# Optimization experiments

Hardware: AMD Instinct MI355X
Metric: run time of the kernel (lower is better)

## Reference

```python
import jax, jax.numpy as jnp
import numpy as np

N = 1_000_000
H = 256
DIMS = [1, H, H, H, H]
N_LAYERS = 4  # 4 linear layers, sin activation after the first 3


def setup_inputs() -> dict:
    key = jax.random.key(0)
    ks = jax.random.split(key, 1 + 2 * N_LAYERS)
    d = {"x": jax.random.normal(ks[0], (N, 2), dtype=jnp.float32)}
    i = 1
    for pre in ("x", "t"):
        for l in range(N_LAYERS):
            lim = 1.0 / np.sqrt(DIMS[l])  # torch.nn.Linear default init range
            d[f"{pre}W{l}"] = jax.random.uniform(
                ks[i], (DIMS[l], DIMS[l + 1]), dtype=jnp.float32, minval=-lim, maxval=lim)
            d[f"{pre}b{l}"] = jnp.zeros((DIMS[l + 1],), dtype=jnp.float32)
            i += 1
    return d


def _mlp(h, params):
    # params: list of (W, b); sin activation after all but the last layer
    n = len(params)
    for idx, (W, b) in enumerate(params):
        h = h @ W + b
        if idx < n - 1:
            h = jnp.sin(h)
    return h


def reference(x, xW0, xb0, xW1, xb1, xW2, xb2, xW3, xb3,
              tW0, tb0, tW1, tb1, tW2, tb2, tW3, tb3):
    x_params = [(xW0, xb0), (xW1, xb1), (xW2, xb2), (xW3, xb3)]
    t_params = [(tW0, tb0), (tW1, tb1), (tW2, tb2), (tW3, tb3)]
    nx = _mlp(x[:, 0:1], x_params)  # [N, H]
    nt = _mlp(x[:, 1:2], t_params)  # [N, H]
    # diag(A @ B.T) == rowwise dot product; avoids the O(N^2) matmul
    even = jnp.sum(nx[:, 0::2] * nt[:, 0::2], axis=-1)  # [N]
    odd = jnp.sum(nx[:, 1::2] * nt[:, 1::2], axis=-1)   # [N]
    return jnp.stack([even, odd], axis=-1)  # [N, 2]
```

## Files before the change

### kernel.cpp

```cpp
#include <hip/hip_runtime.h>


typedef _Float16 f16x8 __attribute__((ext_vector_type(8)));
typedef _Float16 f16x4 __attribute__((ext_vector_type(4)));
typedef float f32x4 __attribute__((ext_vector_type(4)));

__device__ __forceinline__ int hswz(int m, int kbyte) {
    return m * 512 + ((((kbyte >> 4) ^ (m & 7)) & 31) << 4) + (kbyte & 15);
}

__device__ __forceinline__ void barrier_lds() {
    asm volatile("s_waitcnt lgkmcnt(0)" ::: "memory");
    __builtin_amdgcn_s_barrier();
}

__global__ void prepack(const float* __restrict__ xW1, const float* __restrict__ xW2,
                        const float* __restrict__ xW3, const float* __restrict__ tW1,
                        const float* __restrict__ tW2, const float* __restrict__ tW3,
                        _Float16* __restrict__ dst)
{
    int g = blockIdx.x * 256 + threadIdx.x;
    int L = g >> 16;
    int r = g & 65535;
    int j    = r & 7;
    int ln   = (r >> 3) & 15;
    int quad = (r >> 7) & 3;
    int nhi  = (r >> 9) & 15;
    int ks   = (r >> 13) & 1;
    int c    = (r >> 14) & 3;
    const float* W;
    switch (L) {
        case 0: W = xW1; break;
        case 1: W = xW2; break;
        case 2: W = xW3; break;
        case 3: W = tW1; break;
        case 4: W = tW2; break;
        default: W = tW3; break;
    }
    int n = nhi * 16 + ln;
    int k = c * 64 + ks * 32 + quad * 8 + j;
    dst[g] = (_Float16)W[k * 256 + n];
}


__device__ __forceinline__ void layer0_scalar(
    float xv, const float* __restrict__ W0, const float* __restrict__ b0,
    _Float16* __restrict__ hb, int tid)
{
    int m = tid >> 2;
    int q = tid & 3;
#pragma unroll
    for (int g = 0; g < 8; ++g) {
        int n0 = q * 64 + g * 8;
        f16x8 hv;
#pragma unroll
        for (int e = 0; e < 8; ++e) {
            float z = fmaf(xv, W0[n0 + e], b0[n0 + e]);
            hv[e] = (_Float16)__sinf(z);
        }
        *(f16x8*)((char*)hb + hswz(m, n0 * 2)) = hv;
    }
}

template<bool WRITE_H, bool HAS_NEXT>
__device__ __forceinline__ void gemm_layer(
    const _Float16* __restrict__ Wl,
    const _Float16* __restrict__ Wnext,
    const float* __restrict__ bias,
    _Float16* __restrict__ hb,
    f32x4 acc[4][4], f16x8 afr[2][4],
    int lane, int ln, int quad, int wave)
{
    f32x4 zero = {0.f, 0.f, 0.f, 0.f};
#pragma unroll
    for (int i = 0; i < 4; ++i)
#pragma unroll
        for (int j = 0; j < 4; ++j)
            acc[i][j] = zero;

    const _Float16* abase = Wl + wave * 2048 + lane * 8;

#pragma unroll
    for (int g = 0; g < 8; ++g) {
        f16x8 bfr[4];
#pragma unroll
        for (int j = 0; j < 4; ++j)
            bfr[j] = *(const f16x8*)((const char*)hb +
                                     hswz(16 * j + ln, g * 64 + quad * 16));

        __builtin_amdgcn_s_setprio(1);
#pragma unroll
        for (int i = 0; i < 4; ++i)
#pragma unroll
            for (int j = 0; j < 4; ++j)
                acc[i][j] = __builtin_amdgcn_mfma_f32_16x16x32_f16(
                    afr[g & 1][i], bfr[j], acc[i][j], 0, 0, 0);
        __builtin_amdgcn_s_setprio(0);

        if (g < 6) {
#pragma unroll
            for (int i = 0; i < 4; ++i)
                afr[g & 1][i] = *(const f16x8*)(abase + (g + 2) * 8192 + i * 512);
        } else if (HAS_NEXT) {
#pragma unroll
            for (int i = 0; i < 4; ++i)
                afr[g & 1][i] = *(const f16x8*)(Wnext + (g - 6) * 8192 +
                                                wave * 2048 + lane * 8 + i * 512);
        }
    }

    barrier_lds();

    if (WRITE_H) {
#pragma unroll
        for (int i = 0; i < 4; ++i) {
            int nb = wave * 64 + 16 * i + quad * 4;
            f32x4 bv = *(const f32x4*)&bias[nb];
#pragma unroll
            for (int j = 0; j < 4; ++j) {
                f16x4 hv;
                hv[0] = (_Float16)__sinf(acc[i][j][0] + bv[0]);
                hv[1] = (_Float16)__sinf(acc[i][j][1] + bv[1]);
                hv[2] = (_Float16)__sinf(acc[i][j][2] + bv[2]);
                hv[3] = (_Float16)__sinf(acc[i][j][3] + bv[3]);
                *(f16x4*)((char*)hb + hswz(16 * j + ln, nb * 2)) = hv;
            }
        }
        barrier_lds();
    }
}

__global__ __launch_bounds__(256, 2)
void mlp_fused(const float* __restrict__ x,
               const float* __restrict__ xW0, const float* __restrict__ xb0,
               const float* __restrict__ xb1, const float* __restrict__ xb2,
               const float* __restrict__ xb3,
               const float* __restrict__ tW0, const float* __restrict__ tb0,
               const float* __restrict__ tb1, const float* __restrict__ tb2,
               const float* __restrict__ tb3,
               const _Float16* __restrict__ Wp,
               float* __restrict__ out)
{
    __shared__ __align__(16) _Float16 hbuf[64 * 256];
    __shared__ __align__(16) float    params[10 * 256];

    const int tid = threadIdx.x;
    const int lane = tid & 63;
    const int wave = tid >> 6;
    const int ln = lane & 15;
    const int quad = lane >> 4;
    const int row0 = blockIdx.x * 64;

    {
        const float* psrc[10] = {xW0, xb0, tW0, tb0, xb1, xb2, xb3, tb1, tb2, tb3};
#pragma unroll
        for (int s = 0; s < 10; ++s)
            params[s * 256 + tid] = psrc[s][tid];
    }
    const float2 xv2 = ((const float2*)x)[row0 + (tid >> 2)];

    f32x4 xacc[4][4], tacc[4][4];
    f16x8 afr[2][4];

#pragma unroll
    for (int s = 0; s < 2; ++s)
#pragma unroll
        for (int i = 0; i < 4; ++i)
            afr[s][i] = *(const f16x8*)(Wp + s * 8192 + wave * 2048 +
                                        lane * 8 + i * 512);
    barrier_lds();

    layer0_scalar(xv2.x, &params[0], &params[256], hbuf, tid);
    barrier_lds();

    gemm_layer<true , true >(Wp + 0 * 65536, Wp + 1 * 65536, &params[4 * 256],
                             hbuf, xacc, afr, lane, ln, quad, wave);
    gemm_layer<true , true >(Wp + 1 * 65536, Wp + 2 * 65536, &params[5 * 256],
                             hbuf, xacc, afr, lane, ln, quad, wave);
    gemm_layer<false, true >(Wp + 2 * 65536, Wp + 3 * 65536, nullptr,
                             hbuf, xacc, afr, lane, ln, quad, wave);

    layer0_scalar(xv2.y, &params[2 * 256], &params[3 * 256], hbuf, tid);
    barrier_lds();

    gemm_layer<true , true >(Wp + 3 * 65536, Wp + 4 * 65536, &params[7 * 256],
                             hbuf, tacc, afr, lane, ln, quad, wave);
    gemm_layer<true , true >(Wp + 4 * 65536, Wp + 5 * 65536, &params[8 * 256],
                             hbuf, tacc, afr, lane, ln, quad, wave);
    gemm_layer<false, false>(Wp + 5 * 65536, nullptr, nullptr,
                             hbuf, tacc, afr, lane, ln, quad, wave);

    const float* xb3l = &params[6 * 256];
    const float* tb3l = &params[9 * 256];
    float ev[4] = {0.f, 0.f, 0.f, 0.f};
    float od[4] = {0.f, 0.f, 0.f, 0.f};
#pragma unroll
    for (int i = 0; i < 4; ++i) {
        int nb = wave * 64 + 16 * i + quad * 4;
        f32x4 xb = *(const f32x4*)&xb3l[nb];
        f32x4 tb = *(const f32x4*)&tb3l[nb];
#pragma unroll
        for (int j = 0; j < 4; ++j) {
            float a0 = xacc[i][j][0] + xb[0], c0 = tacc[i][j][0] + tb[0];
            float a1 = xacc[i][j][1] + xb[1], c1 = tacc[i][j][1] + tb[1];
            float a2 = xacc[i][j][2] + xb[2], c2 = tacc[i][j][2] + tb[2];
            float a3 = xacc[i][j][3] + xb[3], c3 = tacc[i][j][3] + tb[3];
            ev[j] += a0 * c0 + a2 * c2;
            od[j] += a1 * c1 + a3 * c3;
        }
    }
#pragma unroll
    for (int j = 0; j < 4; ++j) {
        ev[j] += __shfl_xor(ev[j], 16, 64);
        ev[j] += __shfl_xor(ev[j], 32, 64);
        od[j] += __shfl_xor(od[j], 16, 64);
        od[j] += __shfl_xor(od[j], 32, 64);
    }

    float* red = (float*)hbuf;
    if (lane < 16) {
#pragma unroll
        for (int j = 0; j < 4; ++j) {
            red[wave * 128 + j * 32 + lane * 2 + 0] = ev[j];
            red[wave * 128 + j * 32 + lane * 2 + 1] = od[j];
        }
    }
    __syncthreads();
    if (tid < 128) {
        int jj = tid >> 5, m16 = (tid >> 1) & 15, p = tid & 1;
        int base = jj * 32 + m16 * 2 + p;
        float s = red[base] + red[128 + base] + red[256 + base] + red[384 + base];
        out[(row0 + 16 * jj + m16) * 2 + p] = s;
    }
}

extern "C" void kernel_launch(void* const* d_in, const int* in_sizes, int n_in,
                              void* d_out, int out_size, void* d_ws, size_t ws_size,
                              hipStream_t stream)
{
    const float* x   = (const float*)d_in[0];
    const float* xW0 = (const float*)d_in[1];
    const float* xb0 = (const float*)d_in[2];
    const float* xW1 = (const float*)d_in[3];
    const float* xb1 = (const float*)d_in[4];
    const float* xW2 = (const float*)d_in[5];
    const float* xb2 = (const float*)d_in[6];
    const float* xW3 = (const float*)d_in[7];
    const float* xb3 = (const float*)d_in[8];
    const float* tW0 = (const float*)d_in[9];
    const float* tb0 = (const float*)d_in[10];
    const float* tW1 = (const float*)d_in[11];
    const float* tb1 = (const float*)d_in[12];
    const float* tW2 = (const float*)d_in[13];
    const float* tb2 = (const float*)d_in[14];
    const float* tW3 = (const float*)d_in[15];
    const float* tb3 = (const float*)d_in[16];

    _Float16* Wp = (_Float16*)d_ws;
    const int N = in_sizes[0] / 2;

    prepack<<<1536, 256, 0, stream>>>(xW1, xW2, xW3, tW1, tW2, tW3, Wp);
    mlp_fused<<<N / 64, 256, 0, stream>>>(x, xW0, xb0, xb1, xb2, xb3,
                                          tW0, tb0, tb1, tb2, tb3,
                                          Wp, (float*)d_out);
}
```

Baseline: 870.4 us.

## Interleave x and t MLP chains with double-buffered LDS to overlap sin epilogues

The two independent MLP chains are interleaved layer by layer, with the activation buffer double-buffered in LDS. While one chain's GEMM runs on the MFMA units, the other chain's bias+sin epilogue (or its scalar layer-0) is computed and written to the second buffer inside the same k-loop. This hides the transcendental and LDS-write work behind matrix math and removes one barrier per layer. The layer-0 column mapping is also changed, mainly so each k-step can produce its slice. The cost is double the activation LDS per block, which may pressure occupancy, and higher live register usage.

```diff
diff --git a/kernel.cpp b/kernel.cpp
--- a/kernel.cpp
+++ b/kernel.cpp
@@ -51,7 +51,7 @@
     int q = tid & 3;
 #pragma unroll
     for (int g = 0; g < 8; ++g) {
-        int n0 = q * 64 + g * 8;
+        int n0 = g * 32 + q * 8;
         f16x8 hv;
 #pragma unroll
         for (int e = 0; e < 8; ++e) {
@@ -62,14 +62,19 @@
     }
 }
 
-template<bool WRITE_H, bool HAS_NEXT>
-__device__ __forceinline__ void gemm_layer(
+template<int MODE>
+__device__ __forceinline__ void gemm_phase(
     const _Float16* __restrict__ Wl,
     const _Float16* __restrict__ Wnext,
-    const float* __restrict__ bias,
-    _Float16* __restrict__ hb,
+    const _Float16* __restrict__ rb,
     f32x4 acc[4][4], f16x8 afr[2][4],
-    int lane, int ln, int quad, int wave)
+    f32x4 wacc[4][4],
+    const float* __restrict__ wbias,
+    _Float16* __restrict__ wb_lds,
+    float xv,
+    const float* __restrict__ W0,
+    const float* __restrict__ b0,
+    int tid, int lane, int ln, int quad, int wave)
 {
     f32x4 zero = {0.f, 0.f, 0.f, 0.f};
 #pragma unroll
@@ -85,7 +90,7 @@
         f16x8 bfr[4];
 #pragma unroll
         for (int j = 0; j < 4; ++j)
-            bfr[j] = *(const f16x8*)((const char*)hb +
+            bfr[j] = *(const f16x8*)((const char*)rb +
                                      hswz(16 * j + ln, g * 64 + quad * 16));
 
         __builtin_amdgcn_s_setprio(1);
@@ -101,32 +106,38 @@
 #pragma unroll
             for (int i = 0; i < 4; ++i)
                 afr[g & 1][i] = *(const f16x8*)(abase + (g + 2) * 8192 + i * 512);
-        } else if (HAS_NEXT) {
+        } else if (Wnext) {
 #pragma unroll
             for (int i = 0; i < 4; ++i)
                 afr[g & 1][i] = *(const f16x8*)(Wnext + (g - 6) * 8192 +
                                                 wave * 2048 + lane * 8 + i * 512);
         }
-    }
-
-    barrier_lds();
-
-    if (WRITE_H) {
-#pragma unroll
-        for (int i = 0; i < 4; ++i) {
-            int nb = wave * 64 + 16 * i + quad * 4;
-            f32x4 bv = *(const f32x4*)&bias[nb];
-#pragma unroll
-            for (int j = 0; j < 4; ++j) {
+
+        if (MODE == 1) {
+            const int wi = g >> 1;
+            const int nb = wave * 64 + 16 * wi + quad * 4;
+            f32x4 bv = *(const f32x4*)&wbias[nb];
+#pragma unroll
+            for (int jo = 0; jo < 2; ++jo) {
+                const int wj = (g & 1) * 2 + jo;
                 f16x4 hv;
-                hv[0] = (_Float16)__sinf(acc[i][j][0] + bv[0]);
-                hv[1] = (_Float16)__sinf(acc[i][j][1] + bv[1]);
-                hv[2] = (_Float16)__sinf(acc[i][j][2] + bv[2]);
-                hv[3] = (_Float16)__sinf(acc[i][j][3] + bv[3]);
-                *(f16x4*)((char*)hb + hswz(16 * j + ln, nb * 2)) = hv;
+                hv[0] = (_Float16)__sinf(wacc[wi][wj][0] + bv[0]);
+                hv[1] = (_Float16)__sinf(wacc[wi][wj][1] + bv[1]);
+                hv[2] = (_Float16)__sinf(wacc[wi][wj][2] + bv[2]);
+                hv[3] = (_Float16)__sinf(wacc[wi][wj][3] + bv[3]);
+                *(f16x4*)((char*)wb_lds + hswz(16 * wj + ln, nb * 2)) = hv;
             }
-        }
-        barrier_lds();
+        } else if (MODE == 2) {
+            const int m = tid >> 2, q = tid & 3;
+            const int n0 = g * 32 + q * 8;
+            f16x8 hv;
+#pragma unroll
+            for (int e = 0; e < 8; ++e) {
+                float z = fmaf(xv, W0[n0 + e], b0[n0 + e]);
+                hv[e] = (_Float16)__sinf(z);
+            }
+            *(f16x8*)((char*)wb_lds + hswz(m, n0 * 2)) = hv;
+        }
     }
 }
 
@@ -141,7 +152,7 @@
                const _Float16* __restrict__ Wp,
                float* __restrict__ out)
 {
-    __shared__ __align__(16) _Float16 hbuf[64 * 256];
+    __shared__ __align__(16) _Float16 hbuf[2][64 * 256];
     __shared__ __align__(16) float    params[10 * 256];
 
     const int tid = threadIdx.x;
@@ -170,25 +181,33 @@
                                         lane * 8 + i * 512);
     barrier_lds();
 
-    layer0_scalar(xv2.x, &params[0], &params[256], hbuf, tid);
-    barrier_lds();
-
-    gemm_layer<true , true >(Wp + 0 * 65536, Wp + 1 * 65536, &params[4 * 256],
-                             hbuf, xacc, afr, lane, ln, quad, wave);
-    gemm_layer<true , true >(Wp + 1 * 65536, Wp + 2 * 65536, &params[5 * 256],
-                             hbuf, xacc, afr, lane, ln, quad, wave);
-    gemm_layer<false, true >(Wp + 2 * 65536, Wp + 3 * 65536, nullptr,
-                             hbuf, xacc, afr, lane, ln, quad, wave);
-
-    layer0_scalar(xv2.y, &params[2 * 256], &params[3 * 256], hbuf, tid);
-    barrier_lds();
-
-    gemm_layer<true , true >(Wp + 3 * 65536, Wp + 4 * 65536, &params[7 * 256],
-                             hbuf, tacc, afr, lane, ln, quad, wave);
-    gemm_layer<true , true >(Wp + 4 * 65536, Wp + 5 * 65536, &params[8 * 256],
-                             hbuf, tacc, afr, lane, ln, quad, wave);
-    gemm_layer<false, false>(Wp + 5 * 65536, nullptr, nullptr,
-                             hbuf, tacc, afr, lane, ln, quad, wave);
+    layer0_scalar(xv2.x, &params[0], &params[256], hbuf[0], tid);
+    barrier_lds();
+
+    gemm_phase<2>(Wp + 0 * 65536, Wp + 3 * 65536, hbuf[0], xacc, afr,
+                  nullptr, nullptr, hbuf[1],
+                  xv2.y, &params[2 * 256], &params[3 * 256],
+                  tid, lane, ln, quad, wave);
+    barrier_lds();
+    gemm_phase<1>(Wp + 3 * 65536, Wp + 1 * 65536, hbuf[1], tacc, afr,
+                  xacc, &params[4 * 256], hbuf[0],
+                  0.f, nullptr, nullptr, tid, lane, ln, quad, wave);
+    barrier_lds();
+    gemm_phase<1>(Wp + 1 * 65536, Wp + 4 * 65536, hbuf[0], xacc, afr,
+                  tacc, &params[7 * 256], hbuf[1],
+                  0.f, nullptr, nullptr, tid, lane, ln, quad, wave);
+    barrier_lds();
+    gemm_phase<1>(Wp + 4 * 65536, Wp + 2 * 65536, hbuf[1], tacc, afr,
+                  xacc, &params[5 * 256], hbuf[0],
+                  0.f, nullptr, nullptr, tid, lane, ln, quad, wave);
+    barrier_lds();
+    gemm_phase<1>(Wp + 2 * 65536, Wp + 5 * 65536, hbuf[0], xacc, afr,
+                  tacc, &params[8 * 256], hbuf[1],
+                  0.f, nullptr, nullptr, tid, lane, ln, quad, wave);
+    barrier_lds();
+    gemm_phase<0>(Wp + 5 * 65536, nullptr, hbuf[1], tacc, afr,
+                  nullptr, nullptr, nullptr,
+                  0.f, nullptr, nullptr, tid, lane, ln, quad, wave);
 
     const float* xb3l = &params[6 * 256];
     const float* tb3l = &params[9 * 256];
@@ -217,7 +236,7 @@
         od[j] += __shfl_xor(od[j], 32, 64);
     }
 
-    float* red = (float*)hbuf;
+    float* red = (float*)hbuf[0];
     if (lane < 16) {
 #pragma unroll
         for (int j = 0; j < 4; ++j) {
```

New measurement: 855.2 us. No clear change (-1.7%).
